# Performance work log

Hardware: AMD Instinct MI355X
Metric: run time of the kernel (lower is better)

The kernel has to match this reference:

```python
import jax, jax.numpy as jnp
import numpy as np

B, K, D = 32768, 64, 64
GAIN = 1.0
LOG_2PI = float(np.log(2.0 * np.pi))


def setup_inputs() -> dict:
    key = jax.random.key(0)
    k1, k2, k3, k4 = jax.random.split(key, 4)
    return {
        "x": jax.random.normal(k1, (B, D), jnp.float32),
        "means_raw": jax.random.normal(k2, (K, D), jnp.float32),
        "scale_raw": jax.random.normal(k3, (K, D, D), jnp.float32),
        "weights_raw": jax.random.normal(k4, (K,), jnp.float32),
    }


def reference(x, means_raw, scale_raw, weights_raw):
    # EqualizedLR reparametrization: w_eff = w * gain / sqrt(fan_in)
    means = means_raw * (GAIN / np.sqrt(K * D))              # [K, D]
    pre = scale_raw * (GAIN / np.sqrt(K * D * D))            # [K, D, D]
    # ExpScaleTril (diag=False): strict lower triangle + exp(diagonal)
    dvec = jnp.exp(jnp.diagonal(pre, axis1=-2, axis2=-1))    # [K, D]
    L = jnp.tril(pre, -1) + dvec[..., :, None] * jnp.eye(D, dtype=pre.dtype)  # [K, D, D]
    # mixture logits -> log weights (EqualizedLR then softmax parametrization)
    logw = jax.nn.log_softmax(weights_raw * (GAIN / np.sqrt(K)), axis=-1)    # [K]

    # Precompute L^{-1} per component (K,D small), then whiten via one big GEMM.
    eye = jnp.broadcast_to(jnp.eye(D, dtype=L.dtype), L.shape)
    Linv = jax.scipy.linalg.solve_triangular(L, eye, lower=True)             # [K, D, D]

    diff = x[:, None, :] - means[None, :, :]                 # [B, K, D]
    z = jnp.einsum('kij,bkj->bki', Linv, diff)               # whitened residuals [B, K, D]
    maha = jnp.sum(z * z, axis=-1)                           # [B, K]
    half_log_det = jnp.sum(jnp.log(dvec), axis=-1)           # [K]
    comp_lp = -0.5 * (maha + D * LOG_2PI) - half_log_det     # [B, K]

    lp = jax.scipy.special.logsumexp(comp_lp + logw, axis=-1)  # [B]
    return -jnp.mean(lp)
```

## Files before the change

kernel.cpp:

```cpp
#include <hip/hip_runtime.h>

#define LOG_2PI 1.8378770664093453f

typedef __attribute__((ext_vector_type(8))) short  short8;
typedef __attribute__((ext_vector_type(4))) float  float4_;

__device__ __forceinline__ unsigned short f2bf(float f) {
  unsigned u = __builtin_bit_cast(unsigned, f);
  u += 0x7fffu + ((u >> 16) & 1u);
  return (unsigned short)(u >> 16);
}
__device__ __forceinline__ float bf2f(unsigned short h) {
  unsigned u = ((unsigned)h) << 16;
  return __builtin_bit_cast(float, u);
}
template <int CTRL>
__device__ __forceinline__ float dpp_add(float v) {
  int t = __builtin_amdgcn_mov_dpp(__builtin_bit_cast(int, v), CTRL, 0xf, 0xf, true);
  return v + __builtin_bit_cast(float, t);
}
__device__ __forceinline__ void async16(const void* g, void* l) {
  __builtin_amdgcn_global_load_lds((const __attribute__((address_space(1))) unsigned int*)g,
                                   (__attribute__((address_space(3))) unsigned int*)l, 16, 0, 0);
}

__global__ __launch_bounds__(256) void gmm_setup(
    const float* __restrict__ means_raw, const float* __restrict__ scale_raw,
    const float* __restrict__ weights_raw, unsigned short* __restrict__ Wf)
{
  const int k = blockIdx.x;
  const int t = threadIdx.x;
  const int lane = t & 63;
  const int wv = t >> 6;
  const int q = lane >> 4;
  const int jj = lane & 15;

  __shared__ float Plt[64][68];
  __shared__ float Vt[64][68];
  __shared__ __align__(16) unsigned short Vb[64][72];
  __shared__ float dg[64], rdg[64], mu_s[64], y_s[64];

  {
    const int i = t >> 2;
    const int c0 = (t & 3) * 16;
    float4_ v4[4];
    const float4_* src = (const float4_*)(scale_raw + (size_t)k * 4096 + i * 64 + c0);
    v4[0] = src[0]; v4[1] = src[1]; v4[2] = src[2]; v4[3] = src[3];
#pragma unroll
    for (int e = 0; e < 16; ++e) {
      const int c = c0 + e;
      const float val = ((const float*)v4)[e] * (1.0f / 512.0f);
      Plt[c][i] = (c < i) ? val : 0.0f;
      if (c == i) { dg[i] = val; rdg[i] = __expf(-val); }
    }
  }
  if (t < 64) mu_s[t] = means_raw[k * 64 + t] * (1.0f / 64.0f);
  __syncthreads();

  {
    const int j = wv * 16 + jj;
    float s[16];
#pragma unroll
    for (int i = 0; i < 16; ++i) s[i] = 0.0f;
#pragma unroll
    for (int m = 0; m < 64; ++m) {
      const float rm = rdg[m];
      float vcand = (m == j) ? rm : -s[m & 15] * rm;
      const float v = __shfl(vcand, (m >> 4) * 16 + jj, 64);
      if (q == (m >> 4)) {
        Vt[j][m] = v;
        Vb[j][m] = f2bf(v);
      }
      const float4_* prow = (const float4_*)&Plt[m][16 * q];
      const float4_ p0 = prow[0], p1 = prow[1], p2 = prow[2], p3 = prow[3];
      s[0]  += p0[0] * v; s[1]  += p0[1] * v; s[2]  += p0[2] * v; s[3]  += p0[3] * v;
      s[4]  += p1[0] * v; s[5]  += p1[1] * v; s[6]  += p1[2] * v; s[7]  += p1[3] * v;
      s[8]  += p2[0] * v; s[9]  += p2[1] * v; s[10] += p2[2] * v; s[11] += p2[3] * v;
      s[12] += p3[0] * v; s[13] += p3[1] * v; s[14] += p3[2] * v; s[15] += p3[3] * v;
    }
  }
  __syncthreads();

  {
    unsigned short* Wk = Wf + (size_t)k * 4608;
    const short8 a0 = *(const short8*)&Vb[16 * wv + jj][8 * q];
    const short8 a1 = *(const short8*)&Vb[16 * wv + jj][8 * q + 32];
#pragma unroll
    for (int t4 = 0; t4 < 4; ++t4) {
      const short8 b0 = *(const short8*)&Vb[jj + 16 * t4][8 * q];
      const short8 b1 = *(const short8*)&Vb[jj + 16 * t4][8 * q + 32];
      float4_ f = {0.f, 0.f, 0.f, 0.f};
      f = __builtin_amdgcn_mfma_f32_16x16x32_bf16(a0, b0, f, 0, 0, 0);
      f = __builtin_amdgcn_mfma_f32_16x16x32_bf16(a1, b1, f, 0, 0, 0);
#pragma unroll
      for (int r = 0; r < 4; ++r)
        Wk[(16 * wv + 4 * q + r) * 72 + jj + 16 * t4] = f2bf(-0.5f * f[r]);
    }
  }
  if (wv == 0) {
    float acc = 0.0f;
    for (int j2 = 0; j2 < 64; ++j2) acc += Vt[j2][lane] * mu_s[j2];
    y_s[lane] = acc;
  }
  __syncthreads();

  if (t < 64) {
    const int i = t;
    float ci = 0.0f;
#pragma unroll
    for (int m4 = 0; m4 < 16; ++m4) {
      const float4_ a4 = *(const float4_*)&Vt[i][4 * m4];
      const float4_ b4 = *(const float4_*)&y_s[4 * m4];
      ci += a4[0] * b4[0] + a4[1] * b4[1] + a4[2] * b4[2] + a4[3] * b4[3];
    }
    char* Wk = (char*)(Wf + (size_t)k * 4608);
    *(float*)(Wk + i * 144 + 128) = ci;
    float rq  = ci * mu_s[i];
    float dgv = dg[i];
    const float wr = weights_raw[i] * 0.125f;
    float mx = wr;
#pragma unroll
    for (int d = 1; d < 64; d <<= 1) mx = fmaxf(mx, __shfl_xor(mx, d, 64));
    float se = __expf(wr - mx);
#pragma unroll
    for (int d = 1; d < 64; d <<= 1) {
      se  += __shfl_xor(se, d, 64);
      rq  += __shfl_xor(rq, d, 64);
      dgv += __shfl_xor(dgv, d, 64);
    }
    if (i == 0) {
      const float wrk  = weights_raw[k] * 0.125f;
      const float logw = wrk - mx - __logf(se);
      *(float*)(Wk + 132) = -0.5f * rq - 32.0f * LOG_2PI - dgv + logw;
    }
  }
}

__global__ __launch_bounds__(256, 4) void gmm_main(
    const float* __restrict__ x, const unsigned short* __restrict__ Wf,
    unsigned short* __restrict__ ph)
{
  __shared__ __align__(16) unsigned short Wlds[2][2][4608];

  const int t = threadIdx.x;
  const int lane = t & 63;
  const int wv = t >> 6;
  const int q = lane >> 4;
  const int lr = lane & 15;
  const int kh = blockIdx.x & 3;
  const int rt = blockIdx.x >> 2;
  const int rowBase = rt * 128 + wv * 32;
  const int kbase = kh * 16;

  short8 a[2][2];
#pragma unroll
  for (int mt = 0; mt < 2; ++mt)
#pragma unroll
    for (int ks = 0; ks < 2; ++ks) {
      const float4_* xv = (const float4_*)(x + (size_t)(rowBase + mt * 16 + lr) * 64 + ks * 32 + q * 8);
      const float4_ lo = xv[0], hi = xv[1];
      short8 v;
      v[0] = f2bf(lo[0]); v[1] = f2bf(lo[1]); v[2] = f2bf(lo[2]); v[3] = f2bf(lo[3]);
      v[4] = f2bf(hi[0]); v[5] = f2bf(hi[1]); v[6] = f2bf(hi[2]); v[7] = f2bf(hi[3]);
      a[mt][ks] = v;
    }

  float xc[2][4][4];
#pragma unroll
  for (int mt = 0; mt < 2; ++mt)
#pragma unroll
    for (int r = 0; r < 4; ++r) {
      const float* xp = x + (size_t)(rowBase + mt * 16 + q * 4 + r) * 64 + lr;
#pragma unroll
      for (int t4 = 0; t4 < 4; ++t4) xc[mt][t4][r] = xp[16 * t4];
    }

  float sacc[2][4] = {{0, 0, 0, 0}, {0, 0, 0, 0}};

#define STAGE(g, slot)                                                          \
  {                                                                             \
    const unsigned short* src = Wf + (size_t)(kbase + 2 * (g)) * 4608 + t * 8;  \
    unsigned short* dst = &Wlds[slot][0][0] + t * 8;                            \
    async16(src,         dst);                                                  \
    async16(src + 2048,  dst + 2048);                                           \
    async16(src + 4096,  dst + 4096);                                           \
    async16(src + 6144,  dst + 6144);                                           \
    if (t < 128) async16(src + 8192, dst + 8192);                               \
  }

  STAGE(0, 0)
  __syncthreads();

  for (int g = 0; g < 8; ++g) {
    const int cur = g & 1;
    if (g < 7) STAGE(g + 1, cur ^ 1)
#pragma unroll
    for (int kk = 0; kk < 2; ++kk) {
      const unsigned short* wb = &Wlds[cur][kk][0];
      float cc[4];
#pragma unroll
      for (int t4 = 0; t4 < 4; ++t4)
        cc[t4] = *(const float*)(wb + (lr + 16 * t4) * 72 + 64);
      const float bk = *(const float*)(wb + 66) + 90.0f;

      short8 b[2][4];
#pragma unroll
      for (int t4 = 0; t4 < 4; ++t4)
#pragma unroll
        for (int ks = 0; ks < 2; ++ks)
          b[ks][t4] = *(const short8*)(wb + (lr + 16 * t4) * 72 + 8 * q + 32 * ks);

      float4_ f[2][4];
#pragma unroll
      for (int mt = 0; mt < 2; ++mt)
#pragma unroll
        for (int t4 = 0; t4 < 4; ++t4) {
          const float cv = cc[t4];
          float4_ acc = {cv, cv, cv, cv};
          acc = __builtin_amdgcn_mfma_f32_16x16x32_bf16(a[mt][0], b[0][t4], acc, 0, 0, 0);
          acc = __builtin_amdgcn_mfma_f32_16x16x32_bf16(a[mt][1], b[1][t4], acc, 0, 0, 0);
          f[mt][t4] = acc;
        }

#pragma unroll
      for (int mt = 0; mt < 2; ++mt)
#pragma unroll
        for (int r = 0; r < 4; ++r) {
          float sdot = xc[mt][0][r] * f[mt][0][r] + xc[mt][1][r] * f[mt][1][r]
                     + xc[mt][2][r] * f[mt][2][r] + xc[mt][3][r] * f[mt][3][r];
          sdot = dpp_add<0x121>(sdot);
          sdot = dpp_add<0x122>(sdot);
          sdot = dpp_add<0x124>(sdot);
          sdot = dpp_add<0x128>(sdot);
          sacc[mt][r] += __expf(sdot + bk);
        }
    }
    __syncthreads();
  }
#undef STAGE

  if (lr == 0) {
#pragma unroll
    for (int mt = 0; mt < 2; ++mt)
#pragma unroll
      for (int r = 0; r < 4; ++r)
        ph[(size_t)kh * 32768 + rowBase + mt * 16 + q * 4 + r] = f2bf(sacc[mt][r]);
  }
}

__global__ __launch_bounds__(256) void gmm_final1(const unsigned short* __restrict__ ph,
                                                  float* __restrict__ p1)
{
  const int t = threadIdx.x;
  const int r0 = blockIdx.x * 512 + t;
  float v = 0.0f;
#pragma unroll
  for (int h = 0; h < 2; ++h) {
    const int row = r0 + 256 * h;
    const float s = bf2f(ph[row]) + bf2f(ph[32768 + row])
                  + bf2f(ph[65536 + row]) + bf2f(ph[98304 + row]);
    v += __logf(s) - 90.0f;
  }
#pragma unroll
  for (int d = 1; d < 64; d <<= 1) v += __shfl_xor(v, d, 64);
  __shared__ float s4[4];
  if ((t & 63) == 0) s4[t >> 6] = v;
  __syncthreads();
  if (t == 0) p1[blockIdx.x] = s4[0] + s4[1] + s4[2] + s4[3];
}

__global__ __launch_bounds__(64) void gmm_final2(const float* __restrict__ p1,
                                                 float* __restrict__ out)
{
  float v = p1[threadIdx.x];
#pragma unroll
  for (int d = 1; d < 64; d <<= 1) v += __shfl_xor(v, d, 64);
  if (threadIdx.x == 0) out[0] = -v * (1.0f / 32768.0f);
}

extern "C" void kernel_launch(void* const* d_in, const int* in_sizes, int n_in,
                              void* d_out, int out_size, void* d_ws, size_t ws_size,
                              hipStream_t stream)
{
  const float* x           = (const float*)d_in[0];
  const float* means_raw   = (const float*)d_in[1];
  const float* scale_raw   = (const float*)d_in[2];
  const float* weights_raw = (const float*)d_in[3];
  float* out = (float*)d_out;

  char* ws = (char*)d_ws;
  unsigned short* Wf = (unsigned short*)ws;
  unsigned short* ph = (unsigned short*)(ws + 589824);
  float* p1          = (float*)(ws + 851968);

  gmm_setup<<<64, 256, 0, stream>>>(means_raw, scale_raw, weights_raw, Wf);
  gmm_main<<<1024, 256, 0, stream>>>(x, Wf, ph);
  gmm_final1<<<64, 256, 0, stream>>>(ph, p1);
  gmm_final2<<<1, 64, 0, stream>>>(p1, out);
}
```

Baseline: 109.4 us.

## Double rows per block, fold log2e into weights, and merge final reductions

Each wave in the main kernel now handles 64 rows instead of 32, which halves the grid and reuses each staged W tile across twice as many rows. Launch bounds drop to 2 blocks per CU to make room for the extra registers. The setup kernel pre-scales the weights and bias by log2(e) and folds in the +90 offset, so the inner loop calls exp2f with no extra multiply or add. The two final reduction kernels become one kernel that atomically adds into an output zeroed by a memset, which removes a launch but makes the float summation order nondeterministic.

After: 113.3 us. 3.6% more time.

```diff
diff --git a/kernel.cpp b/kernel.cpp
--- a/kernel.cpp
+++ b/kernel.cpp
@@ -1,6 +1,7 @@
 #include <hip/hip_runtime.h>
 
 #define LOG_2PI 1.8378770664093453f
+#define LOG2E   1.4426950408889634f
 
 typedef __attribute__((ext_vector_type(8))) short  short8;
 typedef __attribute__((ext_vector_type(4))) float  float4_;
@@ -94,7 +95,7 @@
       f = __builtin_amdgcn_mfma_f32_16x16x32_bf16(a1, b1, f, 0, 0, 0);
 #pragma unroll
       for (int r = 0; r < 4; ++r)
-        Wk[(16 * wv + 4 * q + r) * 72 + jj + 16 * t4] = f2bf(-0.5f * f[r]);
+        Wk[(16 * wv + 4 * q + r) * 72 + jj + 16 * t4] = f2bf(-0.5f * LOG2E * f[r]);
     }
   }
   if (wv == 0) {
@@ -114,7 +115,7 @@
       ci += a4[0] * b4[0] + a4[1] * b4[1] + a4[2] * b4[2] + a4[3] * b4[3];
     }
     char* Wk = (char*)(Wf + (size_t)k * 4608);
-    *(float*)(Wk + i * 144 + 128) = ci;
+    *(float*)(Wk + i * 144 + 128) = LOG2E * ci;
     float rq  = ci * mu_s[i];
     float dgv = dg[i];
     const float wr = weights_raw[i] * 0.125f;
@@ -131,12 +132,13 @@
     if (i == 0) {
       const float wrk  = weights_raw[k] * 0.125f;
       const float logw = wrk - mx - __logf(se);
-      *(float*)(Wk + 132) = -0.5f * rq - 32.0f * LOG_2PI - dgv + logw;
-    }
-  }
-}
-
-__global__ __launch_bounds__(256, 4) void gmm_main(
+      const float beta = -0.5f * rq - 32.0f * LOG_2PI - dgv + logw;
+      *(float*)(Wk + 132) = LOG2E * (beta + 90.0f);
+    }
+  }
+}
+
+__global__ __launch_bounds__(256, 2) void gmm_main(
     const float* __restrict__ x, const unsigned short* __restrict__ Wf,
     unsigned short* __restrict__ ph)
 {
@@ -149,12 +151,12 @@
   const int lr = lane & 15;
   const int kh = blockIdx.x & 3;
   const int rt = blockIdx.x >> 2;
-  const int rowBase = rt * 128 + wv * 32;
+  const int rowBase = rt * 256 + wv * 64;
   const int kbase = kh * 16;
 
-  short8 a[2][2];
-#pragma unroll
-  for (int mt = 0; mt < 2; ++mt)
+  short8 a[4][2];
+#pragma unroll
+  for (int mt = 0; mt < 4; ++mt)
 #pragma unroll
     for (int ks = 0; ks < 2; ++ks) {
       const float4_* xv = (const float4_*)(x + (size_t)(rowBase + mt * 16 + lr) * 64 + ks * 32 + q * 8);
@@ -165,9 +167,9 @@
       a[mt][ks] = v;
     }
 
-  float xc[2][4][4];
-#pragma unroll
-  for (int mt = 0; mt < 2; ++mt)
+  float xc[4][4][4];
+#pragma unroll
+  for (int mt = 0; mt < 4; ++mt)
 #pragma unroll
     for (int r = 0; r < 4; ++r) {
       const float* xp = x + (size_t)(rowBase + mt * 16 + q * 4 + r) * 64 + lr;
@@ -175,7 +177,7 @@
       for (int t4 = 0; t4 < 4; ++t4) xc[mt][t4][r] = xp[16 * t4];
     }
 
-  float sacc[2][4] = {{0, 0, 0, 0}, {0, 0, 0, 0}};
+  float sacc[4][4] = {{0,0,0,0},{0,0,0,0},{0,0,0,0},{0,0,0,0}};
 
 #define STAGE(g, slot)                                                          \
   {                                                                             \
@@ -201,7 +203,7 @@
 #pragma unroll
       for (int t4 = 0; t4 < 4; ++t4)
         cc[t4] = *(const float*)(wb + (lr + 16 * t4) * 72 + 64);
-      const float bk = *(const float*)(wb + 66) + 90.0f;
+      const float bk = *(const float*)(wb + 66);
 
       short8 b[2][4];
 #pragma unroll
@@ -210,30 +212,34 @@
         for (int ks = 0; ks < 2; ++ks)
           b[ks][t4] = *(const short8*)(wb + (lr + 16 * t4) * 72 + 8 * q + 32 * ks);
 
-      float4_ f[2][4];
-#pragma unroll
-      for (int mt = 0; mt < 2; ++mt)
-#pragma unroll
-        for (int t4 = 0; t4 < 4; ++t4) {
-          const float cv = cc[t4];
-          float4_ acc = {cv, cv, cv, cv};
-          acc = __builtin_amdgcn_mfma_f32_16x16x32_bf16(a[mt][0], b[0][t4], acc, 0, 0, 0);
-          acc = __builtin_amdgcn_mfma_f32_16x16x32_bf16(a[mt][1], b[1][t4], acc, 0, 0, 0);
-          f[mt][t4] = acc;
+#pragma unroll
+      for (int mh = 0; mh < 2; ++mh) {
+        float4_ f[2][4];
+#pragma unroll
+        for (int mi = 0; mi < 2; ++mi)
+#pragma unroll
+          for (int t4 = 0; t4 < 4; ++t4) {
+            const float cv = cc[t4];
+            float4_ acc = {cv, cv, cv, cv};
+            acc = __builtin_amdgcn_mfma_f32_16x16x32_bf16(a[2 * mh + mi][0], b[0][t4], acc, 0, 0, 0);
+            acc = __builtin_amdgcn_mfma_f32_16x16x32_bf16(a[2 * mh + mi][1], b[1][t4], acc, 0, 0, 0);
+            f[mi][t4] = acc;
+          }
+#pragma unroll
+        for (int mi = 0; mi < 2; ++mi) {
+          const int mt = 2 * mh + mi;
+#pragma unroll
+          for (int r = 0; r < 4; ++r) {
+            float sdot = xc[mt][0][r] * f[mi][0][r] + xc[mt][1][r] * f[mi][1][r]
+                       + xc[mt][2][r] * f[mi][2][r] + xc[mt][3][r] * f[mi][3][r];
+            sdot = dpp_add<0x121>(sdot);
+            sdot = dpp_add<0x122>(sdot);
+            sdot = dpp_add<0x124>(sdot);
+            sdot = dpp_add<0x128>(sdot);
+            sacc[mt][r] += exp2f(sdot + bk);
+          }
         }
-
-#pragma unroll
-      for (int mt = 0; mt < 2; ++mt)
-#pragma unroll
-        for (int r = 0; r < 4; ++r) {
-          float sdot = xc[mt][0][r] * f[mt][0][r] + xc[mt][1][r] * f[mt][1][r]
-                     + xc[mt][2][r] * f[mt][2][r] + xc[mt][3][r] * f[mt][3][r];
-          sdot = dpp_add<0x121>(sdot);
-          sdot = dpp_add<0x122>(sdot);
-          sdot = dpp_add<0x124>(sdot);
-          sdot = dpp_add<0x128>(sdot);
-          sacc[mt][r] += __expf(sdot + bk);
-        }
+      }
     }
     __syncthreads();
   }
@@ -241,15 +247,15 @@
 
   if (lr == 0) {
 #pragma unroll
-    for (int mt = 0; mt < 2; ++mt)
+    for (int mt = 0; mt < 4; ++mt)
 #pragma unroll
       for (int r = 0; r < 4; ++r)
         ph[(size_t)kh * 32768 + rowBase + mt * 16 + q * 4 + r] = f2bf(sacc[mt][r]);
   }
 }
 
-__global__ __launch_bounds__(256) void gmm_final1(const unsigned short* __restrict__ ph,
-                                                  float* __restrict__ p1)
+__global__ __launch_bounds__(256) void gmm_final(const unsigned short* __restrict__ ph,
+                                                 float* __restrict__ out)
 {
   const int t = threadIdx.x;
   const int r0 = blockIdx.x * 512 + t;
@@ -266,16 +272,8 @@
   __shared__ float s4[4];
   if ((t & 63) == 0) s4[t >> 6] = v;
   __syncthreads();
-  if (t == 0) p1[blockIdx.x] = s4[0] + s4[1] + s4[2] + s4[3];
-}
-
-__global__ __launch_bounds__(64) void gmm_final2(const float* __restrict__ p1,
-                                                 float* __restrict__ out)
-{
-  float v = p1[threadIdx.x];
-#pragma unroll
-  for (int d = 1; d < 64; d <<= 1) v += __shfl_xor(v, d, 64);
-  if (threadIdx.x == 0) out[0] = -v * (1.0f / 32768.0f);
+  if (t == 0)
+    atomicAdd(out, -(s4[0] + s4[1] + s4[2] + s4[3]) * (1.0f / 32768.0f));
 }
 
 extern "C" void kernel_launch(void* const* d_in, const int* in_sizes, int n_in,
@@ -291,10 +289,9 @@
   char* ws = (char*)d_ws;
   unsigned short* Wf = (unsigned short*)ws;
   unsigned short* ph = (unsigned short*)(ws + 589824);
-  float* p1          = (float*)(ws + 851968);
-
+
+  hipMemsetAsync(out, 0, sizeof(float), stream);
   gmm_setup<<<64, 256, 0, stream>>>(means_raw, scale_raw, weights_raw, Wf);
-  gmm_main<<<1024, 256, 0, stream>>>(x, Wf, ph);
-  gmm_final1<<<64, 256, 0, stream>>>(ph, p1);
-  gmm_final2<<<1, 64, 0, stream>>>(p1, out);
-}
+  gmm_main<<<512, 256, 0, stream>>>(x, Wf, ph);
+  gmm_final<<<64, 256, 0, stream>>>(ph, out);
+}
```
